# Kernel tuning notes

Hardware: AMD Instinct MI355X
Metric: run time of the kernel (lower is better)

Reference implementation:

```python
import jax, jax.numpy as jnp
import numpy as np

ATT_DEPTH = 3
PATCH = 8


def setup_inputs() -> dict:
    key = jax.random.key(0)
    k1, k2 = jax.random.split(key)
    B, C, H, W = 8, 16, 512, 512
    x = jax.random.normal(k1, (B, C, H, W), dtype=jnp.float32)
    L = (H // PATCH) * (W // PATCH)            # 4096 target patches
    Lp = (H // (PATCH * 2 ** ATT_DEPTH)) * (W // (PATCH * 2 ** ATT_DEPTH))  # 64 source patches
    attentions = jax.random.uniform(k2, (B, 1, L, Lp), dtype=jnp.float32)
    return {"x": x, "attentions": attentions}


def reference(x, attentions):
    B, C, H, W = x.shape
    d = 2 ** ATT_DEPTH
    p = PATCH
    # depthwise ones-conv stride d, divided by d*d == average pooling
    argx = x.reshape(B, C, H // d, d, W // d, d).mean(axis=(3, 5))  # [B,C,h,w]
    h, w = H // d, W // d
    hp, wp = h // p, w // p
    # nn.Unfold(kernel=p, stride=p): channels ordered (C, kh, kw), locations row-major
    unf = (argx.reshape(B, C, hp, p, wp, p)
               .transpose(0, 1, 3, 5, 2, 4)
               .reshape(B, C * p * p, hp * wp))  # [B, C*p*p, L']
    # normalize attention rows by nonzero count (non-differentiable int count)
    nz = jax.lax.stop_gradient(
        jnp.count_nonzero(attentions, axis=-1).astype(attentions.dtype)
    )[..., None] + 1e-05  # [B,1,L,1]
    # [B,1,L,L'] @ [B,1,L',C*p*p] -> [B,1,L,C*p*p]
    att = jnp.matmul(attentions / nz, unf[:, None].transpose(0, 1, 3, 2))
    att = jnp.squeeze(att, axis=1).transpose(0, 2, 1)  # [B, C*p*p, L]
    # Fold(output=(H,W), kernel=p, stride=p): non-overlapping -> pure reshape
    Hp, Wp = H // p, W // p
    out = (att.reshape(B, C, p, p, Hp, Wp)
              .transpose(0, 1, 4, 2, 5, 3)
              .reshape(B, C, H, W))
    return out
```

## Files before the change

### kernel.cpp

```cpp
#include <hip/hip_runtime.h>
#include <hip/hip_bf16.h>

typedef __attribute__((ext_vector_type(4))) float f32x4;
typedef __attribute__((ext_vector_type(8))) short s16x8;

#define NB 8
#define NC 16
#define HH 512
#define WW 512

__global__ __launch_bounds__(256) void pool_to_bt(const float* __restrict__ x,
                                                  __hip_bfloat16* __restrict__ bt) {
    int flat = blockIdx.x * 256 + threadIdx.x;
    int wq = flat & 63;
    int hq = (flat >> 6) & 63;
    int c  = (flat >> 12) & 15;
    int b  = flat >> 16;
    const float* base = x + ((size_t)(b * NC + c) * HH + hq * 8) * WW + wq * 8;
    float s = 0.f;
#pragma unroll
    for (int r = 0; r < 8; ++r) {
        f32x4 v0 = *(const f32x4*)(base + (size_t)r * WW);
        f32x4 v1 = *(const f32x4*)(base + (size_t)r * WW + 4);
        s += v0[0] + v0[1] + v0[2] + v0[3] + v1[0] + v1[1] + v1[2] + v1[3];
    }
    s *= (1.f / 64.f);
    int m  = c * 64 + (hq & 7) * 8 + (wq & 7);
    int lp = (hq >> 3) * 8 + (wq >> 3);
    bt[((size_t)b * 1024 + m) * 64 + lp] = __float2bfloat16(s);
}

__global__ __launch_bounds__(256) void attn_prep(const float* __restrict__ attn,
                                                 __hip_bfloat16* __restrict__ abf) {
    int row  = blockIdx.x * 4 + (threadIdx.x >> 6);
    int lane = threadIdx.x & 63;
    float v = attn[(size_t)row * 64 + lane];
    unsigned long long nzmask = __ballot(v != 0.0f);
    float inv = 1.0f / ((float)__popcll(nzmask) + 1e-5f);
    abf[(size_t)row * 64 + lane] = __float2bfloat16(v * inv);
}

#define BM 128
#define BN 128
#define LDK 72

__global__ __launch_bounds__(256) void gemm_scatter(const __hip_bfloat16* __restrict__ abf,
                                                    const __hip_bfloat16* __restrict__ bt,
                                                    float* __restrict__ out) {
    int mb = blockIdx.x;
    int lb = blockIdx.y;
    int b  = blockIdx.z;

    __shared__ __align__(16) unsigned short As[BM][LDK];
    __shared__ __align__(16) unsigned short Bs[BN][LDK];

    int tid = threadIdx.x;
    const unsigned short* Ag = (const unsigned short*)abf + ((size_t)b * 4096 + lb * BM) * 64;
    const unsigned short* Bg = (const unsigned short*)bt  + ((size_t)b * 1024 + mb * BN) * 64;
#pragma unroll
    for (int i = 0; i < 4; ++i) {
        int cid = tid + i * 256;
        int row = cid >> 3, c8 = cid & 7;
        *(s16x8*)&As[row][c8 * 8] = *(const s16x8*)(Ag + row * 64 + c8 * 8);
    }
#pragma unroll
    for (int i = 0; i < 4; ++i) {
        int cid = tid + i * 256;
        int row = cid >> 3, c8 = cid & 7;
        *(s16x8*)&Bs[row][c8 * 8] = *(const s16x8*)(Bg + row * 64 + c8 * 8);
    }
    __syncthreads();

    int w    = tid >> 6;
    int lane = tid & 63;
    int wl   = (w >> 1) * 64;
    int wm   = (w & 1) * 64;
    int lr   = lane & 15;
    int kq   = lane >> 4;

    f32x4 acc[4][4] = {};
#pragma unroll
    for (int ks = 0; ks < 2; ++ks) {
        s16x8 af[4], bfr[4];
#pragma unroll
        for (int i = 0; i < 4; ++i)
            af[i] = *(const s16x8*)&As[wl + i * 16 + lr][ks * 32 + kq * 8];
#pragma unroll
        for (int j = 0; j < 4; ++j)
            bfr[j] = *(const s16x8*)&Bs[wm + j * 16 + lr][ks * 32 + kq * 8];
#pragma unroll
        for (int i = 0; i < 4; ++i)
#pragma unroll
            for (int j = 0; j < 4; ++j)
                acc[i][j] = __builtin_amdgcn_mfma_f32_16x16x32_bf16(af[i], bfr[j], acc[i][j], 0, 0, 0);
    }

#pragma unroll
    for (int i = 0; i < 4; ++i) {
#pragma unroll
        for (int jf = 0; jf < 4; ++jf) {
            int m  = mb * BN + wm + jf * 16 + lr;
            int c  = m >> 6, kh = (m >> 3) & 7, kw = m & 7;
#pragma unroll
            for (int j = 0; j < 4; ++j) {
                int l  = lb * BM + wl + i * 16 + kq * 4 + j;
                int Hp = l >> 6, Wp = l & 63;
                out[(((size_t)(b * NC + c) * HH) + Hp * 8 + kh) * WW + Wp * 8 + kw] = acc[i][jf][j];
            }
        }
    }
}

extern "C" void kernel_launch(void* const* d_in, const int* in_sizes, int n_in,
                              void* d_out, int out_size, void* d_ws, size_t ws_size,
                              hipStream_t stream) {
    const float* x    = (const float*)d_in[0];
    const float* attn = (const float*)d_in[1];
    float* out        = (float*)d_out;

    __hip_bfloat16* bt  = (__hip_bfloat16*)d_ws;
    __hip_bfloat16* abf = (__hip_bfloat16*)((char*)d_ws + (1 << 20));

    pool_to_bt<<<2048, 256, 0, stream>>>(x, bt);
    attn_prep<<<8192, 256, 0, stream>>>(attn, abf);
    dim3 grid(8, 32, 8);
    gemm_scatter<<<grid, 256, 0, stream>>>(abf, bt, out);
}
```

Baseline: 60.75 us.

## Fuse attention normalization into GEMM and vectorize output stores via swapped MFMA operands

Removes the separate attn_prep kernel: each GEMM block now loads fp32 attention rows, counts nonzeros, normalizes and converts to bf16 directly into shared memory. The MFMA operands are swapped so each accumulator holds four consecutive m values, which map to consecutive kw positions, allowing 16-byte vector stores instead of scalar scattered stores. The trade-off is that each attention tile is re-read and renormalized by all 8 mb blocks, in fp32, so there is redundant global traffic and ALU work.

```diff
diff --git a/kernel.cpp b/kernel.cpp
--- a/kernel.cpp
+++ b/kernel.cpp
@@ -30,21 +30,11 @@
     bt[((size_t)b * 1024 + m) * 64 + lp] = __float2bfloat16(s);
 }
 
-__global__ __launch_bounds__(256) void attn_prep(const float* __restrict__ attn,
-                                                 __hip_bfloat16* __restrict__ abf) {
-    int row  = blockIdx.x * 4 + (threadIdx.x >> 6);
-    int lane = threadIdx.x & 63;
-    float v = attn[(size_t)row * 64 + lane];
-    unsigned long long nzmask = __ballot(v != 0.0f);
-    float inv = 1.0f / ((float)__popcll(nzmask) + 1e-5f);
-    abf[(size_t)row * 64 + lane] = __float2bfloat16(v * inv);
-}
-
 #define BM 128
 #define BN 128
 #define LDK 72
 
-__global__ __launch_bounds__(256) void gemm_scatter(const __hip_bfloat16* __restrict__ abf,
+__global__ __launch_bounds__(256) void gemm_scatter(const float* __restrict__ attn,
                                                     const __hip_bfloat16* __restrict__ bt,
                                                     float* __restrict__ out) {
     int mb = blockIdx.x;
@@ -55,58 +45,76 @@
     __shared__ __align__(16) unsigned short Bs[BN][LDK];
 
     int tid = threadIdx.x;
-    const unsigned short* Ag = (const unsigned short*)abf + ((size_t)b * 4096 + lb * BM) * 64;
-    const unsigned short* Bg = (const unsigned short*)bt  + ((size_t)b * 1024 + mb * BN) * 64;
+
+    {
+        int row  = tid >> 1;
+        int half = tid & 1;
+        const float* Arow = attn + ((size_t)(b * 4096 + lb * BM + row)) * 64 + half * 32;
+        f32x4 v[8];
+        int cnt = 0;
 #pragma unroll
-    for (int i = 0; i < 4; ++i) {
-        int cid = tid + i * 256;
-        int row = cid >> 3, c8 = cid & 7;
-        *(s16x8*)&As[row][c8 * 8] = *(const s16x8*)(Ag + row * 64 + c8 * 8);
+        for (int j = 0; j < 8; ++j) {
+            v[j] = *(const f32x4*)(Arow + j * 4);
+            cnt += (v[j][0] != 0.f) + (v[j][1] != 0.f) + (v[j][2] != 0.f) + (v[j][3] != 0.f);
+        }
+        cnt += __shfl_xor(cnt, 1);
+        float inv = 1.0f / ((float)cnt + 1e-5f);
+#pragma unroll
+        for (int j = 0; j < 4; ++j) {
+            s16x8 o;
+#pragma unroll
+            for (int e = 0; e < 8; ++e) {
+                __hip_bfloat16 h = __float2bfloat16(v[j * 2 + (e >> 2)][e & 3] * inv);
+                o[e] = (short)*reinterpret_cast<unsigned short*>(&h);
+            }
+            *(s16x8*)&As[row][half * 32 + j * 8] = o;
+        }
     }
+    {
+        const unsigned short* Bg = (const unsigned short*)bt + ((size_t)b * 1024 + mb * BN) * 64;
 #pragma unroll
-    for (int i = 0; i < 4; ++i) {
-        int cid = tid + i * 256;
-        int row = cid >> 3, c8 = cid & 7;
-        *(s16x8*)&Bs[row][c8 * 8] = *(const s16x8*)(Bg + row * 64 + c8 * 8);
+        for (int i = 0; i < 4; ++i) {
+            int cid = tid + i * 256;
+            int row = cid >> 3, c8 = cid & 7;
+            *(s16x8*)&Bs[row][c8 * 8] = *(const s16x8*)(Bg + row * 64 + c8 * 8);
+        }
     }
     __syncthreads();
 
     int w    = tid >> 6;
     int lane = tid & 63;
+    int wm   = (w & 1) * 64;
     int wl   = (w >> 1) * 64;
-    int wm   = (w & 1) * 64;
     int lr   = lane & 15;
     int kq   = lane >> 4;
 
     f32x4 acc[4][4] = {};
 #pragma unroll
     for (int ks = 0; ks < 2; ++ks) {
-        s16x8 af[4], bfr[4];
+        s16x8 mf[4], lf[4];
 #pragma unroll
         for (int i = 0; i < 4; ++i)
-            af[i] = *(const s16x8*)&As[wl + i * 16 + lr][ks * 32 + kq * 8];
+            mf[i] = *(const s16x8*)&Bs[wm + i * 16 + lr][ks * 32 + kq * 8];
 #pragma unroll
         for (int j = 0; j < 4; ++j)
-            bfr[j] = *(const s16x8*)&Bs[wm + j * 16 + lr][ks * 32 + kq * 8];
+            lf[j] = *(const s16x8*)&As[wl + j * 16 + lr][ks * 32 + kq * 8];
 #pragma unroll
         for (int i = 0; i < 4; ++i)
 #pragma unroll
             for (int j = 0; j < 4; ++j)
-                acc[i][j] = __builtin_amdgcn_mfma_f32_16x16x32_bf16(af[i], bfr[j], acc[i][j], 0, 0, 0);
+                acc[i][j] = __builtin_amdgcn_mfma_f32_16x16x32_bf16(mf[i], lf[j], acc[i][j], 0, 0, 0);
     }
 
 #pragma unroll
-    for (int i = 0; i < 4; ++i) {
+    for (int mi = 0; mi < 4; ++mi) {
+        int m0 = mb * BN + wm + mi * 16 + kq * 4;
+        int c  = m0 >> 6, kh = (m0 >> 3) & 7, kw = m0 & 7;
+        float* obase = out + (((size_t)(b * NC + c) * HH) + kh) * WW + kw;
 #pragma unroll
-        for (int jf = 0; jf < 4; ++jf) {
-            int m  = mb * BN + wm + jf * 16 + lr;
-            int c  = m >> 6, kh = (m >> 3) & 7, kw = m & 7;
-#pragma unroll
-            for (int j = 0; j < 4; ++j) {
-                int l  = lb * BM + wl + i * 16 + kq * 4 + j;
-                int Hp = l >> 6, Wp = l & 63;
-                out[(((size_t)(b * NC + c) * HH) + Hp * 8 + kh) * WW + Wp * 8 + kw] = acc[i][jf][j];
-            }
+        for (int lj = 0; lj < 4; ++lj) {
+            int l  = lb * BM + wl + lj * 16 + lr;
+            int Hp = l >> 6, Wp = l & 63;
+            *(f32x4*)(obase + ((size_t)Hp * 8) * WW + Wp * 8) = acc[mi][lj];
         }
     }
 }
@@ -118,11 +126,9 @@
     const float* attn = (const float*)d_in[1];
     float* out        = (float*)d_out;
 
-    __hip_bfloat16* bt  = (__hip_bfloat16*)d_ws;
-    __hip_bfloat16* abf = (__hip_bfloat16*)((char*)d_ws + (1 << 20));
+    __hip_bfloat16* bt = (__hip_bfloat16*)d_ws;
 
     pool_to_bt<<<2048, 256, 0, stream>>>(x, bt);
-    attn_prep<<<8192, 256, 0, stream>>>(attn, abf);
     dim3 grid(8, 32, 8);
-    gemm_scatter<<<grid, 256, 0, stream>>>(abf, bt, out);
+    gemm_scatter<<<grid, 256, 0, stream>>>(attn, bt, out);
 }
```

After: 56.75 us. 1.07x faster.
